# Kernel tuning notes

Hardware: AMD Instinct MI355X
Metric: run time of the kernel (lower is better)

The kernel has to match this reference:

```python
import jax, jax.numpy as jnp
import numpy as np

N, C, G = 262144, 256, 1024
R = C // 4  # reduction bottleneck


def _linear_w(key, out_dim, in_dim):
    # torch.nn.Linear default init: U(-1/sqrt(in), 1/sqrt(in)), weight shape [out, in]
    bound = 1.0 / np.sqrt(in_dim)
    return jax.random.uniform(key, (out_dim, in_dim), jnp.float32, -bound, bound)


def setup_inputs() -> dict:
    key = jax.random.key(0)
    ks = jax.random.split(key, 8)
    return {
        "x": jax.random.normal(ks[0], (N, C), jnp.float32),
        "glb_w1": _linear_w(ks[1], R, C),
        "glb_a": jnp.full((1,), 0.25, jnp.float32),   # PReLU param (default init 0.25)
        "glb_w2": _linear_w(ks[2], C, R),
        "local_w1": _linear_w(ks[3], R, C),
        "local_a": jnp.full((1,), 0.25, jnp.float32),
        "local_w2": _linear_w(ks[4], C, R),
        "attn_w1": _linear_w(ks[5], R, C),
        "attn_a": jnp.full((1,), 0.25, jnp.float32),
        "attn_w2": _linear_w(ks[6], C, R),
        "batch_idx": jnp.sort(jax.random.randint(ks[7], (N,), 0, G)),
        "num_graphs": G,
    }


def _mlp(h, w1, a, w2):
    # Linear(no bias) -> PReLU -> Linear(no bias)
    z = jnp.einsum('nc,rc->nr', h, w1)
    z = jnp.where(z >= 0, z, a * z)
    return jnp.einsum('nr,cr->nc', z, w2)


def reference(x, glb_w1, glb_a, glb_w2, local_w1, local_a, local_w2,
              attn_w1, attn_a, attn_w2, batch_idx, num_graphs):
    g = _mlp(x, glb_w1, glb_a, glb_w2)                                  # [N, C]
    seg_sum = jax.ops.segment_sum(g, batch_idx, num_segments=num_graphs)  # [G, C]
    cnt = jax.ops.segment_sum(jnp.ones((x.shape[0], 1), x.dtype), batch_idx,
                              num_segments=num_graphs)                  # [G, 1]
    seg_mean = seg_sum / jnp.maximum(cnt, 1.0)  # scatter_mean (0 for empty graphs)
    x_glb = seg_mean[batch_idx]                                          # gather back [N, C]
    loc = _mlp(x, local_w1, local_a, local_w2)                           # [N, C]
    attn = _mlp(loc + x_glb, attn_w1, attn_a, attn_w2)
    return jax.nn.sigmoid(attn)
```

## Files before the change

### kernel.cpp

```cpp
#include <hip/hip_runtime.h>

typedef unsigned short u16;
typedef __attribute__((ext_vector_type(8))) short short8;
typedef __attribute__((ext_vector_type(4))) float f32x4;
typedef __attribute__((ext_vector_type(4))) unsigned short u16x4;
typedef __attribute__((ext_vector_type(2))) unsigned u32x2;

#define NN 262144
#define CC 256
#define RR 64
#define GG 1024

#define SWZ(b, n) ((b) ^ (((n) & 7) << 4))


static __device__ __forceinline__ u16 f2bf(float f) {
  unsigned u = __builtin_bit_cast(unsigned, f);
  u += 0x7fffu + ((u >> 16) & 1u);
  return (u16)(u >> 16);
}

static __device__ __forceinline__ unsigned cvt_pk_bf16(float lo, float hi) {
  unsigned r;
  asm("v_cvt_pk_bf16_f32 %0, %1, %2" : "=v"(r) : "v"(lo), "v"(hi));
  return r;
}

static __device__ __forceinline__ void lgkm0() {
  __asm__ volatile("s_waitcnt lgkmcnt(0)" ::: "memory");
}

#define MFMA16(a, b, c) __builtin_amdgcn_mfma_f32_16x16x32_bf16((a), (b), (c), 0, 0, 0)

__global__ void k_cvt(const float* __restrict__ a0, const float* __restrict__ a1,
                      const float* __restrict__ a2, const float* __restrict__ a3,
                      const float* __restrict__ a4, const float* __restrict__ a5,
                      u16* __restrict__ dst) {
  int m = blockIdx.x >> 4;
  const float* s = (m == 0) ? a0 : (m == 1) ? a1 : (m == 2) ? a2
                 : (m == 3) ? a3 : (m == 4) ? a4 : a5;
  int off = (((blockIdx.x & 15) << 8) | threadIdx.x) << 2;
  f32x4 v = *(const f32x4*)(s + off);
  u16x4 p;
  p[0] = f2bf(v[0]); p[1] = f2bf(v[1]); p[2] = f2bf(v[2]); p[3] = f2bf(v[3]);
  *(u16x4*)(dst + m * 16384 + off) = p;
}

#define ZBOFF 32768

__global__ __launch_bounds__(256, 3) void k_glb(
    const float* __restrict__ x, const u16* __restrict__ wbf,
    const int* __restrict__ bidx, const float* __restrict__ pa,
    float* __restrict__ seg, int* __restrict__ cnt) {
  __shared__ __align__(16) char smem[41216];
  const int tid = threadIdx.x;
  const int wave = tid >> 6, lane = tid & 63;
  const int low = lane & 15, quad = lane >> 4;
  const int node0 = blockIdx.x << 6;
  const float alpha = pa[0];
  const u16* w1 = wbf;
  const u16* w2 = wbf + 16384;
  int* lbp = (int*)(smem + 40960);

  if (tid < 64) lbp[tid] = bidx[node0 + tid];

  const float* xsrc = x + (size_t)node0 * CC;
#pragma unroll
  for (int k = 0; k < 16; k++) {
    int f = k * 1024 + tid * 4;
    f32x4 v = *(const f32x4*)(xsrc + f);
    int node = f >> 8;
    u32x2 p;
    p[0] = cvt_pk_bf16(v[0], v[1]);
    p[1] = cvt_pk_bf16(v[2], v[3]);
    *(u32x2*)(smem + SWZ(node * 512 + (f & 255) * 2, node)) = p;
  }
  __syncthreads();

  f32x4 z[4] = {};
  const u16* w1p = w1 + (wave * 16 + low) * CC;
#pragma unroll
  for (int ks = 0; ks < 8; ks++) {
    short8 wa = *(const short8*)(w1p + ks * 32 + quad * 8);
#pragma unroll
    for (int nt = 0; nt < 4; nt++) {
      int node = nt * 16 + low;
      short8 xf = *(const short8*)(smem + SWZ(node * 512 + ks * 64 + quad * 16, node));
      z[nt] = MFMA16(wa, xf, z[nt]);
    }
  }
#pragma unroll
  for (int nt = 0; nt < 4; nt++) {
    float v0 = z[nt][0], v1 = z[nt][1], v2 = z[nt][2], v3 = z[nt][3];
    v0 = v0 >= 0.f ? v0 : alpha * v0;
    v1 = v1 >= 0.f ? v1 : alpha * v1;
    v2 = v2 >= 0.f ? v2 : alpha * v2;
    v3 = v3 >= 0.f ? v3 : alpha * v3;
    int node = nt * 16 + low;
    u32x2 p;
    p[0] = cvt_pk_bf16(v0, v1);
    p[1] = cvt_pk_bf16(v2, v3);
    *(u32x2*)(smem + ZBOFF + SWZ(node * 128 + wave * 32 + quad * 8, node)) = p;
  }
  __syncthreads();

  if (lane == 0) {
    int base = wave * 16;
    int cur = lbp[base], rl = 0;
#pragma unroll
    for (int n = 0; n < 16; n++) {
      int b = lbp[base + n];
      if (b != cur) { atomicAdd(cnt + cur, rl); rl = 0; cur = b; }
      rl++;
    }
    atomicAdd(cnt + cur, rl);
  }

  f32x4 g[4][4] = {};
#pragma unroll
  for (int ks2 = 0; ks2 < 2; ks2++) {
    short8 zf[4];
#pragma unroll
    for (int nt = 0; nt < 4; nt++) {
      int node = nt * 16 + low;
      zf[nt] = *(const short8*)(smem + ZBOFF + SWZ(node * 128 + ks2 * 64 + quad * 16, node));
    }
#pragma unroll
    for (int mt = 0; mt < 4; mt++) {
      short8 wa = *(const short8*)(w2 + (wave * 64 + mt * 16 + low) * RR + ks2 * 32 + quad * 8);
#pragma unroll
      for (int nt = 0; nt < 4; nt++)
        g[nt][mt] = MFMA16(wa, zf[nt], g[nt][mt]);
    }
  }
  lgkm0();

  float* slab = (float*)(smem + wave * 4352);
#pragma unroll
  for (int nt = 0; nt < 4; nt++) {
#pragma unroll
    for (int mt = 0; mt < 4; mt++)
      *(f32x4*)(slab + low * 68 + mt * 16 + quad * 4) = g[nt][mt];
    lgkm0();
    float acc = 0.f;
    int cur = lbp[nt * 16];
#pragma unroll
    for (int n = 0; n < 16; n++) {
      int b = lbp[nt * 16 + n];
      if (b != cur) {
        atomicAdd(seg + (size_t)cur * CC + wave * 64 + lane, acc);
        acc = 0.f; cur = b;
      }
      acc += slab[n * 68 + lane];
    }
    atomicAdd(seg + (size_t)cur * CC + wave * 64 + lane, acc);
    lgkm0();
  }
}

__global__ __launch_bounds__(256) void k_norm(float* __restrict__ seg,
                                              const int* __restrict__ cnt) {
  int g = blockIdx.x;
  int c = cnt[g];
  float s = (c > 0) ? (1.0f / (float)c) : 0.0f;
  seg[(size_t)g * CC + threadIdx.x] *= s;
}

__global__ __launch_bounds__(256, 4) void k_attn(
    const float* __restrict__ x, const u16* __restrict__ wbf,
    const int* __restrict__ bidx, const float* __restrict__ seg,
    const float* __restrict__ pal, const float* __restrict__ paa,
    float* __restrict__ out) {
  __shared__ __align__(16) char smem[40960];
  const int tid = threadIdx.x;
  const int wave = tid >> 6, lane = tid & 63;
  const int low = lane & 15, quad = lane >> 4;
  const int node0 = blockIdx.x << 6;
  const float al = pal[0], aa = paa[0];
  const u16* w1l = wbf + 2 * 16384;
  const u16* w2l = wbf + 3 * 16384;
  const u16* w1a = wbf + 4 * 16384;
  const u16* w2a = wbf + 5 * 16384;

  const float* xsrc = x + (size_t)node0 * CC;
#pragma unroll
  for (int k = 0; k < 16; k++) {
    int f = k * 1024 + tid * 4;
    f32x4 v = *(const f32x4*)(xsrc + f);
    int node = f >> 8;
    u32x2 p;
    p[0] = cvt_pk_bf16(v[0], v[1]);
    p[1] = cvt_pk_bf16(v[2], v[3]);
    *(u32x2*)(smem + SWZ(node * 512 + (f & 255) * 2, node)) = p;
  }
  __syncthreads();

  f32x4 z[4] = {};
  const u16* w1p = w1l + (wave * 16 + low) * CC;
#pragma unroll
  for (int ks = 0; ks < 8; ks++) {
    short8 wa = *(const short8*)(w1p + ks * 32 + quad * 8);
#pragma unroll
    for (int nt = 0; nt < 4; nt++) {
      int node = nt * 16 + low;
      short8 xf = *(const short8*)(smem + SWZ(node * 512 + ks * 64 + quad * 16, node));
      z[nt] = MFMA16(wa, xf, z[nt]);
    }
  }
#pragma unroll
  for (int nt = 0; nt < 4; nt++) {
    float v0 = z[nt][0], v1 = z[nt][1], v2 = z[nt][2], v3 = z[nt][3];
    v0 = v0 >= 0.f ? v0 : al * v0;
    v1 = v1 >= 0.f ? v1 : al * v1;
    v2 = v2 >= 0.f ? v2 : al * v2;
    v3 = v3 >= 0.f ? v3 : al * v3;
    int node = nt * 16 + low;
    u32x2 p;
    p[0] = cvt_pk_bf16(v0, v1);
    p[1] = cvt_pk_bf16(v2, v3);
    *(u32x2*)(smem + ZBOFF + SWZ(node * 128 + wave * 32 + quad * 8, node)) = p;
  }
  __syncthreads();

  f32x4 loc[4][4] = {};
#pragma unroll
  for (int ks2 = 0; ks2 < 2; ks2++) {
    short8 zf[4];
#pragma unroll
    for (int nt = 0; nt < 4; nt++) {
      int node = nt * 16 + low;
      zf[nt] = *(const short8*)(smem + ZBOFF + SWZ(node * 128 + ks2 * 64 + quad * 16, node));
    }
#pragma unroll
    for (int mt = 0; mt < 4; mt++) {
      short8 wa = *(const short8*)(w2l + (wave * 64 + mt * 16 + low) * RR + ks2 * 32 + quad * 8);
#pragma unroll
      for (int nt = 0; nt < 4; nt++)
        loc[nt][mt] = MFMA16(wa, zf[nt], loc[nt][mt]);
    }
  }

  int bb[4];
#pragma unroll
  for (int nt = 0; nt < 4; nt++) bb[nt] = bidx[node0 + nt * 16 + low];
#pragma unroll
  for (int nt = 0; nt < 4; nt++) {
    const float* srow = seg + (size_t)bb[nt] * CC + wave * 64;
    int node = nt * 16 + low;
#pragma unroll
    for (int mt = 0; mt < 4; mt++) {
      f32x4 sv = *(const f32x4*)(srow + mt * 16 + quad * 4);
      u32x2 p;
      p[0] = cvt_pk_bf16(loc[nt][mt][0] + sv[0], loc[nt][mt][1] + sv[1]);
      p[1] = cvt_pk_bf16(loc[nt][mt][2] + sv[2], loc[nt][mt][3] + sv[3]);
      *(u32x2*)(smem + SWZ(node * 512 + wave * 128 + mt * 32 + quad * 8, node)) = p;
    }
  }
  __syncthreads();

  f32x4 z2[4] = {};
  const u16* w1pa = w1a + (wave * 16 + low) * CC;
#pragma unroll
  for (int ks = 0; ks < 8; ks++) {
    short8 wa = *(const short8*)(w1pa + ks * 32 + quad * 8);
#pragma unroll
    for (int nt = 0; nt < 4; nt++) {
      int node = nt * 16 + low;
      short8 hf = *(const short8*)(smem + SWZ(node * 512 + ks * 64 + quad * 16, node));
      z2[nt] = MFMA16(wa, hf, z2[nt]);
    }
  }
#pragma unroll
  for (int nt = 0; nt < 4; nt++) {
    float v0 = z2[nt][0], v1 = z2[nt][1], v2 = z2[nt][2], v3 = z2[nt][3];
    v0 = v0 >= 0.f ? v0 : aa * v0;
    v1 = v1 >= 0.f ? v1 : aa * v1;
    v2 = v2 >= 0.f ? v2 : aa * v2;
    v3 = v3 >= 0.f ? v3 : aa * v3;
    int node = nt * 16 + low;
    u32x2 p;
    p[0] = cvt_pk_bf16(v0, v1);
    p[1] = cvt_pk_bf16(v2, v3);
    *(u32x2*)(smem + ZBOFF + SWZ(node * 128 + wave * 32 + quad * 8, node)) = p;
  }
  __syncthreads();

  f32x4 o[4][4] = {};
#pragma unroll
  for (int ks2 = 0; ks2 < 2; ks2++) {
    short8 zf[4];
#pragma unroll
    for (int nt = 0; nt < 4; nt++) {
      int node = nt * 16 + low;
      zf[nt] = *(const short8*)(smem + ZBOFF + SWZ(node * 128 + ks2 * 64 + quad * 16, node));
    }
#pragma unroll
    for (int mt = 0; mt < 4; mt++) {
      short8 wa = *(const short8*)(w2a + (wave * 64 + mt * 16 + low) * RR + ks2 * 32 + quad * 8);
#pragma unroll
      for (int nt = 0; nt < 4; nt++)
        o[nt][mt] = MFMA16(wa, zf[nt], o[nt][mt]);
    }
  }
#pragma unroll
  for (int nt = 0; nt < 4; nt++)
#pragma unroll
    for (int mt = 0; mt < 4; mt++)
#pragma unroll
      for (int i = 0; i < 4; i++)
        o[nt][mt][i] = __builtin_amdgcn_rcpf(1.0f + __expf(-o[nt][mt][i]));
  lgkm0();

  float* slab = (float*)(smem + wave * 4352);
#pragma unroll
  for (int nt = 0; nt < 4; nt++) {
#pragma unroll
    for (int mt = 0; mt < 4; mt++)
      *(f32x4*)(slab + low * 68 + mt * 16 + quad * 4) = o[nt][mt];
    lgkm0();
#pragma unroll
    for (int n = 0; n < 16; n++)
      out[(size_t)(node0 + nt * 16 + n) * CC + wave * 64 + lane] = slab[n * 68 + lane];
    lgkm0();
  }
}

extern "C" void kernel_launch(void* const* d_in, const int* in_sizes, int n_in,
                              void* d_out, int out_size, void* d_ws, size_t ws_size,
                              hipStream_t stream) {
  (void)in_sizes; (void)n_in; (void)out_size; (void)ws_size;
  const float* x   = (const float*)d_in[0];
  const float* w1g = (const float*)d_in[1];
  const float* ag  = (const float*)d_in[2];
  const float* w2g = (const float*)d_in[3];
  const float* w1l = (const float*)d_in[4];
  const float* al  = (const float*)d_in[5];
  const float* w2l = (const float*)d_in[6];
  const float* w1a = (const float*)d_in[7];
  const float* aa  = (const float*)d_in[8];
  const float* w2a = (const float*)d_in[9];
  const int* bidx  = (const int*)d_in[10];
  float* out = (float*)d_out;

  u16* wbf   = (u16*)d_ws;
  float* seg = (float*)((char*)d_ws + 196608);
  int* cnt   = (int*)((char*)d_ws + 196608 + 1048576);

  hipMemsetAsync(seg, 0, 1048576 + 4096, stream);
  k_cvt<<<96, 256, 0, stream>>>(w1g, w2g, w1l, w2l, w1a, w2a, wbf);
  k_glb<<<NN / 64, 256, 0, stream>>>(x, wbf, bidx, ag, seg, cnt);
  k_norm<<<GG, 256, 0, stream>>>(seg, cnt);
  k_attn<<<NN / 64, 256, 0, stream>>>(x, wbf, bidx, seg, al, aa, out);
}
```

Measured before the change: 649.4 us.

## Alias LDS buffers to raise occupancy and fold segment-mean normalization into attn kernel

Both main kernels now reuse the x-tile LDS region for the bottleneck activations instead of a separate offset, shrinking shared memory from about 40KB to 32KB. Launch bounds rise to 5 blocks per CU, and extra barriers guard the aliased regions. The separate k_norm launch is removed: k_attn loads per-node counts and multiplies the segment sums by a reciprocal with an fma. In exchange it adds more __syncthreads and tighter register budgets, which may cause spills.

```diff
diff --git a/kernel.cpp b/kernel.cpp
--- a/kernel.cpp
+++ b/kernel.cpp
@@ -46,13 +46,12 @@
   *(u16x4*)(dst + m * 16384 + off) = p;
 }
 
-#define ZBOFF 32768
-
-__global__ __launch_bounds__(256, 3) void k_glb(
+
+__global__ __launch_bounds__(256, 5) void k_glb(
     const float* __restrict__ x, const u16* __restrict__ wbf,
     const int* __restrict__ bidx, const float* __restrict__ pa,
     float* __restrict__ seg, int* __restrict__ cnt) {
-  __shared__ __align__(16) char smem[41216];
+  __shared__ __align__(16) char smem[32768];
   const int tid = threadIdx.x;
   const int wave = tid >> 6, lane = tid & 63;
   const int low = lane & 15, quad = lane >> 4;
@@ -60,9 +59,8 @@
   const float alpha = pa[0];
   const u16* w1 = wbf;
   const u16* w2 = wbf + 16384;
-  int* lbp = (int*)(smem + 40960);
-
-  if (tid < 64) lbp[tid] = bidx[node0 + tid];
+
+  int myb_lb = (tid < 64) ? bidx[node0 + tid] : 0;
 
   const float* xsrc = x + (size_t)node0 * CC;
 #pragma unroll
@@ -89,6 +87,9 @@
       z[nt] = MFMA16(wa, xf, z[nt]);
     }
   }
+  __syncthreads();
+
+  if (tid < 64) ((int*)(smem + 20480))[tid] = myb_lb;
 #pragma unroll
   for (int nt = 0; nt < 4; nt++) {
     float v0 = z[nt][0], v1 = z[nt][1], v2 = z[nt][2], v3 = z[nt][3];
@@ -100,9 +101,11 @@
     u32x2 p;
     p[0] = cvt_pk_bf16(v0, v1);
     p[1] = cvt_pk_bf16(v2, v3);
-    *(u32x2*)(smem + ZBOFF + SWZ(node * 128 + wave * 32 + quad * 8, node)) = p;
-  }
-  __syncthreads();
+    *(u32x2*)(smem + SWZ(node * 128 + wave * 32 + quad * 8, node)) = p;
+  }
+  __syncthreads();
+
+  const int* lbp = (const int*)(smem + 20480);
 
   if (lane == 0) {
     int base = wave * 16;
@@ -123,7 +126,7 @@
 #pragma unroll
     for (int nt = 0; nt < 4; nt++) {
       int node = nt * 16 + low;
-      zf[nt] = *(const short8*)(smem + ZBOFF + SWZ(node * 128 + ks2 * 64 + quad * 16, node));
+      zf[nt] = *(const short8*)(smem + SWZ(node * 128 + ks2 * 64 + quad * 16, node));
     }
 #pragma unroll
     for (int mt = 0; mt < 4; mt++) {
@@ -133,7 +136,7 @@
         g[nt][mt] = MFMA16(wa, zf[nt], g[nt][mt]);
     }
   }
-  lgkm0();
+  __syncthreads();
 
   float* slab = (float*)(smem + wave * 4352);
 #pragma unroll
@@ -158,20 +161,13 @@
   }
 }
 
-__global__ __launch_bounds__(256) void k_norm(float* __restrict__ seg,
-                                              const int* __restrict__ cnt) {
-  int g = blockIdx.x;
-  int c = cnt[g];
-  float s = (c > 0) ? (1.0f / (float)c) : 0.0f;
-  seg[(size_t)g * CC + threadIdx.x] *= s;
-}
-
-__global__ __launch_bounds__(256, 4) void k_attn(
+__global__ __launch_bounds__(256, 5) void k_attn(
     const float* __restrict__ x, const u16* __restrict__ wbf,
     const int* __restrict__ bidx, const float* __restrict__ seg,
+    const int* __restrict__ cnt,
     const float* __restrict__ pal, const float* __restrict__ paa,
     float* __restrict__ out) {
-  __shared__ __align__(16) char smem[40960];
+  __shared__ __align__(16) char smem[32768];
   const int tid = threadIdx.x;
   const int wave = tid >> 6, lane = tid & 63;
   const int low = lane & 15, quad = lane >> 4;
@@ -182,6 +178,13 @@
   const u16* w1a = wbf + 4 * 16384;
   const u16* w2a = wbf + 5 * 16384;
 
+  int bb[4];
+#pragma unroll
+  for (int nt = 0; nt < 4; nt++) bb[nt] = bidx[node0 + nt * 16 + low];
+  int cc[4];
+#pragma unroll
+  for (int nt = 0; nt < 4; nt++) cc[nt] = cnt[bb[nt]];
+
   const float* xsrc = x + (size_t)node0 * CC;
 #pragma unroll
   for (int k = 0; k < 16; k++) {
@@ -207,6 +210,7 @@
       z[nt] = MFMA16(wa, xf, z[nt]);
     }
   }
+  __syncthreads();
 #pragma unroll
   for (int nt = 0; nt < 4; nt++) {
     float v0 = z[nt][0], v1 = z[nt][1], v2 = z[nt][2], v3 = z[nt][3];
@@ -218,7 +222,7 @@
     u32x2 p;
     p[0] = cvt_pk_bf16(v0, v1);
     p[1] = cvt_pk_bf16(v2, v3);
-    *(u32x2*)(smem + ZBOFF + SWZ(node * 128 + wave * 32 + quad * 8, node)) = p;
+    *(u32x2*)(smem + SWZ(node * 128 + wave * 32 + quad * 8, node)) = p;
   }
   __syncthreads();
 
@@ -229,7 +233,7 @@
 #pragma unroll
     for (int nt = 0; nt < 4; nt++) {
       int node = nt * 16 + low;
-      zf[nt] = *(const short8*)(smem + ZBOFF + SWZ(node * 128 + ks2 * 64 + quad * 16, node));
+      zf[nt] = *(const short8*)(smem + SWZ(node * 128 + ks2 * 64 + quad * 16, node));
     }
 #pragma unroll
     for (int mt = 0; mt < 4; mt++) {
@@ -239,20 +243,21 @@
         loc[nt][mt] = MFMA16(wa, zf[nt], loc[nt][mt]);
     }
   }
-
-  int bb[4];
-#pragma unroll
-  for (int nt = 0; nt < 4; nt++) bb[nt] = bidx[node0 + nt * 16 + low];
+  __syncthreads();
+
 #pragma unroll
   for (int nt = 0; nt < 4; nt++) {
     const float* srow = seg + (size_t)bb[nt] * CC + wave * 64;
+    float inv = (cc[nt] > 0) ? __builtin_amdgcn_rcpf((float)cc[nt]) : 0.0f;
     int node = nt * 16 + low;
 #pragma unroll
     for (int mt = 0; mt < 4; mt++) {
       f32x4 sv = *(const f32x4*)(srow + mt * 16 + quad * 4);
       u32x2 p;
-      p[0] = cvt_pk_bf16(loc[nt][mt][0] + sv[0], loc[nt][mt][1] + sv[1]);
-      p[1] = cvt_pk_bf16(loc[nt][mt][2] + sv[2], loc[nt][mt][3] + sv[3]);
+      p[0] = cvt_pk_bf16(fmaf(sv[0], inv, loc[nt][mt][0]),
+                         fmaf(sv[1], inv, loc[nt][mt][1]));
+      p[1] = cvt_pk_bf16(fmaf(sv[2], inv, loc[nt][mt][2]),
+                         fmaf(sv[3], inv, loc[nt][mt][3]));
       *(u32x2*)(smem + SWZ(node * 512 + wave * 128 + mt * 32 + quad * 8, node)) = p;
     }
   }
@@ -270,6 +275,7 @@
       z2[nt] = MFMA16(wa, hf, z2[nt]);
     }
   }
+  __syncthreads();
 #pragma unroll
   for (int nt = 0; nt < 4; nt++) {
     float v0 = z2[nt][0], v1 = z2[nt][1], v2 = z2[nt][2], v3 = z2[nt][3];
@@ -281,7 +287,7 @@
     u32x2 p;
     p[0] = cvt_pk_bf16(v0, v1);
     p[1] = cvt_pk_bf16(v2, v3);
-    *(u32x2*)(smem + ZBOFF + SWZ(node * 128 + wave * 32 + quad * 8, node)) = p;
+    *(u32x2*)(smem + SWZ(node * 128 + wave * 32 + quad * 8, node)) = p;
   }
   __syncthreads();
 
@@ -292,7 +298,7 @@
 #pragma unroll
     for (int nt = 0; nt < 4; nt++) {
       int node = nt * 16 + low;
-      zf[nt] = *(const short8*)(smem + ZBOFF + SWZ(node * 128 + ks2 * 64 + quad * 16, node));
+      zf[nt] = *(const short8*)(smem + SWZ(node * 128 + ks2 * 64 + quad * 16, node));
     }
 #pragma unroll
     for (int mt = 0; mt < 4; mt++) {
@@ -309,7 +315,7 @@
 #pragma unroll
       for (int i = 0; i < 4; i++)
         o[nt][mt][i] = __builtin_amdgcn_rcpf(1.0f + __expf(-o[nt][mt][i]));
-  lgkm0();
+  __syncthreads();
 
   float* slab = (float*)(smem + wave * 4352);
 #pragma unroll
@@ -349,6 +355,5 @@
   hipMemsetAsync(seg, 0, 1048576 + 4096, stream);
   k_cvt<<<96, 256, 0, stream>>>(w1g, w2g, w1l, w2l, w1a, w2a, wbf);
   k_glb<<<NN / 64, 256, 0, stream>>>(x, wbf, bidx, ag, seg, cnt);
-  k_norm<<<GG, 256, 0, stream>>>(seg, cnt);
-  k_attn<<<NN / 64, 256, 0, stream>>>(x, wbf, bidx, seg, al, aa, out);
-}
+  k_attn<<<NN / 64, 256, 0, stream>>>(x, wbf, bidx, seg, cnt, al, aa, out);
+}
```

Result: slower. 732.3 us (+12.8%).
